# Kernel tuning notes

Measured on AMD Instinct MI355X. Metric: run time of the kernel, lower is better.

The kernel has to match this reference:

```python
import jax, jax.numpy as jnp
import numpy as np

EPS_ROT = 1e-6
EPS_FRAME = 1e-8


def make_rotX(angs):
    # angs: [..., 2] (cos-like, sin-like); returns [..., 4, 4]
    n = jnp.sqrt(jnp.sum(angs * angs, axis=-1)) + EPS_ROT
    c = angs[..., 0] / n
    s = angs[..., 1] / n
    z = jnp.zeros_like(c)
    o = jnp.ones_like(c)
    rows = jnp.stack([o, z, z, z,
                      z, c, -s, z,
                      z, s, c, z,
                      z, z, z, o], axis=-1)
    return rows.reshape(c.shape + (4, 4))


def make_rotZ(angs):
    n = jnp.sqrt(jnp.sum(angs * angs, axis=-1)) + EPS_ROT
    c = angs[..., 0] / n
    s = angs[..., 1] / n
    z = jnp.zeros_like(c)
    o = jnp.ones_like(c)
    rows = jnp.stack([c, -s, z, z,
                      s, c, z, z,
                      z, z, o, z,
                      z, z, z, o], axis=-1)
    return rows.reshape(c.shape + (4, 4))


def make_rot_axis(angs, u):
    # Rodrigues rotation about unit axis u, as homogeneous 4x4
    n = jnp.sqrt(jnp.sum(angs * angs, axis=-1)) + EPS_ROT
    ct = angs[..., 0] / n
    st = angs[..., 1] / n
    u0, u1, u2 = u[..., 0], u[..., 1], u[..., 2]
    omc = 1.0 - ct
    z = jnp.zeros_like(ct)
    o = jnp.ones_like(ct)
    rows = jnp.stack([
        ct + u0 * u0 * omc, u0 * u1 * omc - u2 * st, u0 * u2 * omc + u1 * st, z,
        u0 * u1 * omc + u2 * st, ct + u1 * u1 * omc, u1 * u2 * omc - u0 * st, z,
        u0 * u2 * omc - u1 * st, u1 * u2 * omc + u0 * st, ct + u2 * u2 * omc, z,
        z, z, z, o], axis=-1)
    return rows.reshape(ct.shape + (4, 4))


def rigid_from_3_points(N, Ca, C):
    # Gram-Schmidt backbone frame (ideal geometry branch)
    v1 = C - Ca
    v2 = N - Ca
    e1 = v1 / (jnp.linalg.norm(v1, axis=-1, keepdims=True) + EPS_FRAME)
    u2 = v2 - e1 * jnp.sum(e1 * v2, axis=-1, keepdims=True)
    e2 = u2 / (jnp.linalg.norm(u2, axis=-1, keepdims=True) + EPS_FRAME)
    e3 = jnp.cross(e1, e2)
    R = jnp.stack([e1, e2, e3], axis=-1)  # columns -> [B,L,3,3]
    return R, Ca


def _compute(seq, xyz, alphas, base_indices, RTs_in_base_frame, xyzs_in_base_frame):
    B, L = xyz.shape[:2]
    Rs, Ts = rigid_from_3_points(xyz[..., 0, :], xyz[..., 1, :], xyz[..., 2, :])
    top = jnp.concatenate([Rs, Ts[..., None]], axis=-1)  # [B,L,3,4]
    bot = jnp.broadcast_to(jnp.array([0.0, 0.0, 0.0, 1.0], dtype=xyz.dtype), (B, L, 1, 4))
    RTF0 = jnp.concatenate([top, bot], axis=-2)  # [B,L,4,4]

    RT_base = RTs_in_base_frame[seq]  # [B,L,7,4,4]

    RTF1 = RTF0 @ RT_base[:, :, 0] @ make_rotX(alphas[:, :, 0, :])
    RTF2 = RTF0 @ RT_base[:, :, 1] @ make_rotX(alphas[:, :, 1, :])
    RTF3 = RTF0 @ RT_base[:, :, 2] @ make_rotX(alphas[:, :, 2, :])

    basexyzs = xyzs_in_base_frame[seq]  # [B,L,36,4]
    NCr = 0.5 * (basexyzs[:, :, 2, :3] + basexyzs[:, :, 0, :3])
    CAr = basexyzs[:, :, 1, :3]
    CBr = basexyzs[:, :, 4, :3]
    ax1 = jnp.cross(CBr - CAr, NCr - CAr)
    ax1 = ax1 / (jnp.linalg.norm(ax1, axis=-1, keepdims=True) + 1e-8)
    NCp = basexyzs[:, :, 2, :3] - basexyzs[:, :, 0, :3]
    NCpp = NCp - jnp.sum(NCp * NCr, axis=-1, keepdims=True) / jnp.sum(NCr * NCr, axis=-1, keepdims=True) * NCr
    ax2 = jnp.cross(CBr - CAr, NCpp)
    ax2 = ax2 / (jnp.linalg.norm(ax2, axis=-1, keepdims=True) + 1e-8)

    CBrot1 = make_rot_axis(alphas[:, :, 7, :], ax1)
    CBrot2 = make_rot_axis(alphas[:, :, 8, :], ax2)
    RTF8 = RTF0 @ CBrot1 @ CBrot2

    RTF4 = RTF8 @ RT_base[:, :, 3] @ make_rotX(alphas[:, :, 3, :]) @ make_rotZ(alphas[:, :, 9, :])
    RTF5 = RTF4 @ RT_base[:, :, 4] @ make_rotX(alphas[:, :, 4, :])
    RTF6 = RTF5 @ RT_base[:, :, 5] @ make_rotX(alphas[:, :, 5, :])
    RTF7 = RTF6 @ RT_base[:, :, 6] @ make_rotX(alphas[:, :, 6, :])

    RTframes = jnp.stack([RTF0, RTF1, RTF2, RTF3, RTF4, RTF5, RTF6, RTF7, RTF8], axis=2)  # [B,L,9,4,4]

    idx = base_indices[seq]  # [B,L,36], values in [0,9)
    frames = jnp.take_along_axis(RTframes, idx[..., None, None], axis=2)  # [B,L,36,4,4]
    xyzs = jnp.einsum('blaij,blaj->blai', frames, basexyzs)
    return RTframes, xyzs[..., :3]


def setup_inputs() -> dict:
    key = jax.random.key(0)
    ks = jax.random.split(key, 6)
    B, L, NAA, NATOMS = 4, 8192, 80, 36
    seq = jax.random.randint(ks[0], (B, L), 0, NAA)
    xyz = jax.random.normal(ks[1], (B, L, 3, 3), jnp.float32)
    alphas = jax.random.normal(ks[2], (B, L, 10, 2), jnp.float32)
    base_indices = jax.random.randint(ks[3], (NAA, NATOMS), 0, 9)
    xibf = jax.random.normal(ks[4], (NAA, NATOMS, 4), jnp.float32)
    xibf = xibf.at[..., 3].set(1.0)  # homogeneous coords
    RTs = jax.random.normal(ks[5], (NAA, 7, 4, 4), jnp.float32)
    return {"seq": seq, "xyz": xyz, "alphas": alphas, "base_indices": base_indices,
            "RTs_in_base_frame": RTs, "xyzs_in_base_frame": xibf}


def reference(seq, xyz, alphas, base_indices, RTs_in_base_frame, xyzs_in_base_frame):
    return _compute(seq, xyz, alphas, base_indices, RTs_in_base_frame, xyzs_in_base_frame)
```

## Files before the change

### kernel.cpp

```cpp
#include <hip/hip_runtime.h>

#define EPS_ROT   1e-6f
#define EPS_FRAME 1e-8f

#define RPB 64
#define FRS 20
#define RSS (9*FRS)
#define PSTR 36


__device__ __forceinline__ void angNorm(float x, float y, float& c, float& s) {
    float n = sqrtf(x*x + y*y) + EPS_ROT;
    c = x / n; s = y / n;
}

__device__ __forceinline__ void loadMat4(const float* __restrict__ p, float B[4][4]) {
    const float4* q = reinterpret_cast<const float4*>(p);
#pragma unroll
    for (int i = 0; i < 4; ++i) {
        float4 r = q[i];
        B[i][0] = r.x; B[i][1] = r.y; B[i][2] = r.z; B[i][3] = r.w;
    }
}

__device__ __forceinline__ void storeMatLDS(float* dst, const float M[4][4]) {
#pragma unroll
    for (int i = 0; i < 4; ++i)
        *reinterpret_cast<float4*>(dst + i*4) = make_float4(M[i][0], M[i][1], M[i][2], M[i][3]);
}

__device__ __forceinline__ void affineMul(const float a[3][4], const float B[4][4], float C[4][4]) {
#pragma unroll
    for (int i = 0; i < 3; ++i)
#pragma unroll
        for (int j = 0; j < 4; ++j)
            C[i][j] = a[i][0]*B[0][j] + a[i][1]*B[1][j] + a[i][2]*B[2][j] + a[i][3]*B[3][j];
#pragma unroll
    for (int j = 0; j < 4; ++j) C[3][j] = B[3][j];
}

__device__ __forceinline__ void mat4Mul(const float A[4][4], const float B[4][4], float C[4][4]) {
#pragma unroll
    for (int i = 0; i < 4; ++i)
#pragma unroll
        for (int j = 0; j < 4; ++j)
            C[i][j] = A[i][0]*B[0][j] + A[i][1]*B[1][j] + A[i][2]*B[2][j] + A[i][3]*B[3][j];
}

__device__ __forceinline__ void postRotX(float M[4][4], float c, float s) {
#pragma unroll
    for (int i = 0; i < 4; ++i) {
        float m1 = M[i][1], m2 = M[i][2];
        M[i][1] = c*m1 + s*m2;
        M[i][2] = c*m2 - s*m1;
    }
}

__device__ __forceinline__ void rotAxis3(float G[3][3], float c, float s,
                                         float u0, float u1, float u2) {
    float omc = 1.0f - c;
    G[0][0] = c + u0*u0*omc;    G[0][1] = u0*u1*omc - u2*s; G[0][2] = u0*u2*omc + u1*s;
    G[1][0] = u0*u1*omc + u2*s; G[1][1] = c + u1*u1*omc;    G[1][2] = u1*u2*omc - u0*s;
    G[2][0] = u0*u2*omc - u1*s; G[2][1] = u1*u2*omc + u0*s; G[2][2] = c + u2*u2*omc;
}

__device__ __forceinline__ void mat3Mul(const float A[3][3], const float B[3][3], float C[3][3]) {
#pragma unroll
    for (int i = 0; i < 3; ++i)
#pragma unroll
        for (int j = 0; j < 3; ++j)
            C[i][j] = A[i][0]*B[0][j] + A[i][1]*B[1][j] + A[i][2]*B[2][j];
}

__device__ __forceinline__ void computeF0(const float* __restrict__ xyz, int t, float f0[3][4]) {
    const float* p = xyz + (size_t)t * 9;
    float N0=p[0], N1=p[1], N2=p[2];
    float A0=p[3], A1=p[4], A2=p[5];
    float C0=p[6], C1=p[7], C2=p[8];

    float v10=C0-A0, v11=C1-A1, v12=C2-A2;
    float v20=N0-A0, v21=N1-A1, v22=N2-A2;
    float n1 = sqrtf(v10*v10 + v11*v11 + v12*v12) + EPS_FRAME;
    float e10=v10/n1, e11=v11/n1, e12=v12/n1;
    float d  = e10*v20 + e11*v21 + e12*v22;
    float u20=v20-e10*d, u21=v21-e11*d, u22=v22-e12*d;
    float n2 = sqrtf(u20*u20 + u21*u21 + u22*u22) + EPS_FRAME;
    float e20=u20/n2, e21=u21/n2, e22=u22/n2;
    float e30=e11*e22 - e12*e21;
    float e31=e12*e20 - e10*e22;
    float e32=e10*e21 - e11*e20;

    f0[0][0]=e10; f0[0][1]=e20; f0[0][2]=e30; f0[0][3]=A0;
    f0[1][0]=e11; f0[1][1]=e21; f0[1][2]=e31; f0[1][3]=A1;
    f0[2][0]=e12; f0[2][1]=e22; f0[2][2]=e32; f0[2][3]=A2;
}


__global__ __launch_bounds__(256) void fused_kernel(
    const int*   __restrict__ seq,
    const float* __restrict__ xyz,
    const float* __restrict__ alphas,
    const int*   __restrict__ bidx,
    const float* __restrict__ RTs,
    const float* __restrict__ xibf,
    float*       __restrict__ out_fr,
    float*       __restrict__ out_xyz,
    int BL)
{
    __shared__ float lds_fr[RPB * RSS];
    __shared__ float lds_P[RPB * PSTR];
    __shared__ int   lds_seq[RPB];

    const int tid = threadIdx.x;
    const int wv  = tid >> 6;
    const int r   = tid & 63;
    const int base = blockIdx.x * RPB;
    const int t   = base + r;
    const bool valid = (t < BL);

    int s = 0;
    if (valid) s = seq[t];
    const float* rb = RTs + (size_t)s * 112;
    const float* al = alphas + (size_t)t * 20;
    float* fl = lds_fr + r * RSS;

    float f8[3][4];
    float P6[4][4], P7[4][4];

    if (valid) {
        if (wv == 0) {
            lds_seq[r] = s;
            float f0[3][4]; computeF0(xyz, t, f0);
            float F0[4][4] = { {f0[0][0],f0[0][1],f0[0][2],f0[0][3]},
                               {f0[1][0],f0[1][1],f0[1][2],f0[1][3]},
                               {f0[2][0],f0[2][1],f0[2][2],f0[2][3]},
                               {0.f,0.f,0.f,1.f} };
            storeMatLDS(fl + 0*FRS, F0);

            float2 a0 = *reinterpret_cast<const float2*>(al + 0);
            float c0, s0; angNorm(a0.x, a0.y, c0, s0);
            float B[4][4]; loadMat4(rb + 0, B);
            float F[4][4]; affineMul(f0, B, F); postRotX(F, c0, s0);
            storeMatLDS(fl + 1*FRS, F);
        } else if (wv == 1) {
            float f0[3][4]; computeF0(xyz, t, f0);
            float2 a1 = *reinterpret_cast<const float2*>(al + 2);
            float2 a2 = *reinterpret_cast<const float2*>(al + 4);
            float c, sn;
            float B[4][4], F[4][4];
            angNorm(a1.x, a1.y, c, sn);
            loadMat4(rb + 16, B); affineMul(f0, B, F); postRotX(F, c, sn);
            storeMatLDS(fl + 2*FRS, F);
            angNorm(a2.x, a2.y, c, sn);
            loadMat4(rb + 32, B); affineMul(f0, B, F); postRotX(F, c, sn);
            storeMatLDS(fl + 3*FRS, F);
        } else if (wv == 2) {
            float f0[3][4]; computeF0(xyz, t, f0);
            const float* bxp = xibf + (size_t)s * 144;
            float4 b0 = reinterpret_cast<const float4*>(bxp)[0];
            float4 b1 = reinterpret_cast<const float4*>(bxp)[1];
            float4 b2 = reinterpret_cast<const float4*>(bxp)[2];
            float4 b4 = reinterpret_cast<const float4*>(bxp)[4];

            float NCr0 = 0.5f*(b2.x + b0.x), NCr1 = 0.5f*(b2.y + b0.y), NCr2 = 0.5f*(b2.z + b0.z);
            float ba0 = b4.x - b1.x, ba1 = b4.y - b1.y, ba2 = b4.z - b1.z;
            float w0 = NCr0 - b1.x, w1 = NCr1 - b1.y, w2 = NCr2 - b1.z;
            float x10 = ba1*w2 - ba2*w1, x11 = ba2*w0 - ba0*w2, x12 = ba0*w1 - ba1*w0;
            float xn1 = sqrtf(x10*x10 + x11*x11 + x12*x12) + 1e-8f;
            x10 /= xn1; x11 /= xn1; x12 /= xn1;
            float NCp0 = b2.x - b0.x, NCp1 = b2.y - b0.y, NCp2 = b2.z - b0.z;
            float dp = NCp0*NCr0 + NCp1*NCr1 + NCp2*NCr2;
            float dr = NCr0*NCr0 + NCr1*NCr1 + NCr2*NCr2;
            float sf = dp / dr;
            float q0 = NCp0 - sf*NCr0, q1 = NCp1 - sf*NCr1, q2 = NCp2 - sf*NCr2;
            float x20 = ba1*q2 - ba2*q1, x21 = ba2*q0 - ba0*q2, x22 = ba0*q1 - ba1*q0;
            float xn2 = sqrtf(x20*x20 + x21*x21 + x22*x22) + 1e-8f;
            x20 /= xn2; x21 /= xn2; x22 /= xn2;

            float2 a7 = *reinterpret_cast<const float2*>(al + 14);
            float2 a8 = *reinterpret_cast<const float2*>(al + 16);
            float c7, s7, c8, s8;
            angNorm(a7.x, a7.y, c7, s7);
            angNorm(a8.x, a8.y, c8, s8);
            float G1[3][3], G2[3][3], G12[3][3], R8[3][3];
            rotAxis3(G1, c7, s7, x10, x11, x12);
            rotAxis3(G2, c8, s8, x20, x21, x22);
            mat3Mul(G1, G2, G12);
            float R0[3][3] = { {f0[0][0],f0[0][1],f0[0][2]},
                               {f0[1][0],f0[1][1],f0[1][2]},
                               {f0[2][0],f0[2][1],f0[2][2]} };
            mat3Mul(R0, G12, R8);
#pragma unroll
            for (int i = 0; i < 3; ++i) {
                f8[i][0] = R8[i][0]; f8[i][1] = R8[i][1]; f8[i][2] = R8[i][2];
                f8[i][3] = f0[i][3];
            }
            float F8[4][4] = { {f8[0][0],f8[0][1],f8[0][2],f8[0][3]},
                               {f8[1][0],f8[1][1],f8[1][2],f8[1][3]},
                               {f8[2][0],f8[2][1],f8[2][2],f8[2][3]},
                               {0.f,0.f,0.f,1.f} };
            storeMatLDS(fl + 8*FRS, F8);
        } else {
            float2 a3 = *reinterpret_cast<const float2*>(al + 6);
            float2 a4 = *reinterpret_cast<const float2*>(al + 8);
            float2 a5 = *reinterpret_cast<const float2*>(al + 10);
            float2 a6 = *reinterpret_cast<const float2*>(al + 12);
            float2 a9 = *reinterpret_cast<const float2*>(al + 18);
            float c3,s3, c4,s4, c5,s5, c6,s6, c9,s9;
            angNorm(a3.x, a3.y, c3, s3);
            angNorm(a4.x, a4.y, c4, s4);
            angNorm(a5.x, a5.y, c5, s5);
            angNorm(a6.x, a6.y, c6, s6);
            angNorm(a9.x, a9.y, c9, s9);

            float M00 = c9,     M01 = -s9;
            float M10 = c3*s9,  M11 = c3*c9,  M12 = -s3;
            float M20 = s3*s9,  M21 = s3*c9,  M22 = c3;

            float B[4][4]; loadMat4(rb + 48, B);
            float P4[4][4];
#pragma unroll
            for (int i = 0; i < 4; ++i) {
                P4[i][0] = B[i][0]*M00 + B[i][1]*M10 + B[i][2]*M20;
                P4[i][1] = B[i][0]*M01 + B[i][1]*M11 + B[i][2]*M21;
                P4[i][2] =               B[i][1]*M12 + B[i][2]*M22;
                P4[i][3] = B[i][3];
            }
            float P5[4][4];
            loadMat4(rb + 64, B); mat4Mul(P4, B, P5); postRotX(P5, c4, s4);
            loadMat4(rb + 80, B); mat4Mul(P5, B, P6); postRotX(P6, c5, s5);
            loadMat4(rb + 96, B); mat4Mul(P6, B, P7); postRotX(P7, c6, s6);

            float* pl = lds_P + r * PSTR;
            storeMatLDS(pl,      P4);
            storeMatLDS(pl + 16, P5);
        }
    }
    __syncthreads();

    if (valid) {
        if (wv == 2) {
            const float* pl = lds_P + r * PSTR;
            float P[4][4], F[4][4];
            loadMat4(pl, P);
            affineMul(f8, P, F); storeMatLDS(fl + 4*FRS, F);
            loadMat4(pl + 16, P);
            affineMul(f8, P, F); storeMatLDS(fl + 5*FRS, F);
        } else if (wv == 3) {
            float f8b[3][4];
            const float* q = fl + 8*FRS;
#pragma unroll
            for (int i = 0; i < 3; ++i) {
                float4 v = *reinterpret_cast<const float4*>(q + i*4);
                f8b[i][0] = v.x; f8b[i][1] = v.y; f8b[i][2] = v.z; f8b[i][3] = v.w;
            }
            float F[4][4];
            affineMul(f8b, P6, F); storeMatLDS(fl + 6*FRS, F);
            affineMul(f8b, P7, F); storeMatLDS(fl + 7*FRS, F);
        }
    }
    __syncthreads();

    for (int c = tid; c < RPB*36; c += 256) {
        int res = c / 36;
        int q = c - res*36;
        int tt = base + res;
        if (tt < BL) {
            float4 v = *reinterpret_cast<const float4*>(
                lds_fr + res*RSS + (q >> 2)*FRS + (q & 3)*4);
            *reinterpret_cast<float4*>(out_fr + (size_t)tt*144 + q*4) = v;
        }
    }

    for (int c = tid; c < RPB*36; c += 256) {
        int res = c / 36;
        int a = c - res*36;
        int tt = base + res;
        if (tt < BL) {
            int ss = lds_seq[res];
            int idx = bidx[ss*36 + a];
            const float* fp = lds_fr + res*RSS + idx*FRS;
            float4 r0 = *reinterpret_cast<const float4*>(fp);
            float4 r1 = *reinterpret_cast<const float4*>(fp + 4);
            float4 r2 = *reinterpret_cast<const float4*>(fp + 8);
            float4 v  = *reinterpret_cast<const float4*>(xibf + ((size_t)ss*36 + a)*4);
            size_t o = (size_t)tt*108 + (size_t)a*3;
            out_xyz[o+0] = r0.x*v.x + r0.y*v.y + r0.z*v.z + r0.w*v.w;
            out_xyz[o+1] = r1.x*v.x + r1.y*v.y + r1.z*v.z + r1.w*v.w;
            out_xyz[o+2] = r2.x*v.x + r2.y*v.y + r2.z*v.z + r2.w*v.w;
        }
    }
}


extern "C" void kernel_launch(void* const* d_in, const int* in_sizes, int n_in,
                              void* d_out, int out_size, void* d_ws, size_t ws_size,
                              hipStream_t stream) {
    const int*   seq    = (const int*)  d_in[0];
    const float* xyz    = (const float*)d_in[1];
    const float* alphas = (const float*)d_in[2];
    const int*   bidx   = (const int*)  d_in[3];
    const float* RTs    = (const float*)d_in[4];
    const float* xibf   = (const float*)d_in[5];
    float*       out    = (float*)d_out;

    int BL = in_sizes[0];
    float* out_xyz = out + (size_t)BL * 144;

    int blocks = (BL + RPB - 1) / RPB;
    fused_kernel<<<blocks, 256, 0, stream>>>(seq, xyz, alphas, bidx, RTs, xibf,
                                             out, out_xyz, BL);
}
```

Before: 16.54 us.

## Coalesce xyz output stores, shrink LDS frame stride, use rsqrt normalization

Rewrites the atom-coordinate write loop so each thread produces one output float, giving contiguous coalesced stores instead of three strided scalar writes per thread. It also stores both output arrays with nontemporal stores and shrinks the per-frame LDS stride from 20 to 18 floats, which forces float2 LDS accesses. The P4/P5 staging buffer is dropped so wave 3 computes all four composed frames itself, and launch bounds request 3 blocks per CU. Normalizations switch from sqrt-plus-epsilon divides to a clamped rsqrt, which changes the epsilon semantics slightly and may cause small numerical differences.

```diff
diff --git a/kernel.cpp b/kernel.cpp
--- a/kernel.cpp
+++ b/kernel.cpp
@@ -1,32 +1,44 @@
 #include <hip/hip_runtime.h>
 
-#define EPS_ROT   1e-6f
-#define EPS_FRAME 1e-8f
-
 #define RPB 64
-#define FRS 20
+#define FRS 18
 #define RSS (9*FRS)
-#define PSTR 36
-
+
+typedef float __attribute__((ext_vector_type(4))) fvec4;
+
+
+__device__ __forceinline__ float rsqz(float d) { return rsqrtf(fmaxf(d, 1e-24f)); }
 
 __device__ __forceinline__ void angNorm(float x, float y, float& c, float& s) {
-    float n = sqrtf(x*x + y*y) + EPS_ROT;
-    c = x / n; s = y / n;
+    float inv = rsqz(x*x + y*y);
+    c = x * inv; s = y * inv;
 }
 
 __device__ __forceinline__ void loadMat4(const float* __restrict__ p, float B[4][4]) {
-    const float4* q = reinterpret_cast<const float4*>(p);
+    const float4* q4 = reinterpret_cast<const float4*>(p);
 #pragma unroll
     for (int i = 0; i < 4; ++i) {
-        float4 r = q[i];
-        B[i][0] = r.x; B[i][1] = r.y; B[i][2] = r.z; B[i][3] = r.w;
-    }
+        float4 r = q4[i];
+        B[i][0]=r.x; B[i][1]=r.y; B[i][2]=r.z; B[i][3]=r.w;
+    }
+}
+
+__device__ __forceinline__ void storeRowLDS(float* dst, float a, float b, float c, float d) {
+    *reinterpret_cast<float2*>(dst)     = make_float2(a, b);
+    *reinterpret_cast<float2*>(dst + 2) = make_float2(c, d);
 }
 
 __device__ __forceinline__ void storeMatLDS(float* dst, const float M[4][4]) {
 #pragma unroll
     for (int i = 0; i < 4; ++i)
-        *reinterpret_cast<float4*>(dst + i*4) = make_float4(M[i][0], M[i][1], M[i][2], M[i][3]);
+        storeRowLDS(dst + i*4, M[i][0], M[i][1], M[i][2], M[i][3]);
+}
+
+__device__ __forceinline__ void storeAffineLDS(float* dst, const float f[3][4]) {
+#pragma unroll
+    for (int i = 0; i < 3; ++i)
+        storeRowLDS(dst + i*4, f[i][0], f[i][1], f[i][2], f[i][3]);
+    storeRowLDS(dst + 12, 0.f, 0.f, 0.f, 1.f);
 }
 
 __device__ __forceinline__ void affineMul(const float a[3][4], const float B[4][4], float C[4][4]) {
@@ -80,12 +92,12 @@
 
     float v10=C0-A0, v11=C1-A1, v12=C2-A2;
     float v20=N0-A0, v21=N1-A1, v22=N2-A2;
-    float n1 = sqrtf(v10*v10 + v11*v11 + v12*v12) + EPS_FRAME;
-    float e10=v10/n1, e11=v11/n1, e12=v12/n1;
+    float i1 = rsqz(v10*v10 + v11*v11 + v12*v12);
+    float e10=v10*i1, e11=v11*i1, e12=v12*i1;
     float d  = e10*v20 + e11*v21 + e12*v22;
     float u20=v20-e10*d, u21=v21-e11*d, u22=v22-e12*d;
-    float n2 = sqrtf(u20*u20 + u21*u21 + u22*u22) + EPS_FRAME;
-    float e20=u20/n2, e21=u21/n2, e22=u22/n2;
+    float i2 = rsqz(u20*u20 + u21*u21 + u22*u22);
+    float e20=u20*i2, e21=u21*i2, e22=u22*i2;
     float e30=e11*e22 - e12*e21;
     float e31=e12*e20 - e10*e22;
     float e32=e10*e21 - e11*e20;
@@ -96,7 +108,7 @@
 }
 
 
-__global__ __launch_bounds__(256) void fused_kernel(
+__global__ __launch_bounds__(256, 3) void fused_kernel(
     const int*   __restrict__ seq,
     const float* __restrict__ xyz,
     const float* __restrict__ alphas,
@@ -108,14 +120,13 @@
     int BL)
 {
     __shared__ float lds_fr[RPB * RSS];
-    __shared__ float lds_P[RPB * PSTR];
     __shared__ int   lds_seq[RPB];
 
-    const int tid = threadIdx.x;
-    const int wv  = tid >> 6;
-    const int r   = tid & 63;
+    const int tid  = threadIdx.x;
+    const int wv   = tid >> 6;
+    const int r    = tid & 63;
     const int base = blockIdx.x * RPB;
-    const int t   = base + r;
+    const int t    = base + r;
     const bool valid = (t < BL);
 
     int s = 0;
@@ -124,23 +135,19 @@
     const float* al = alphas + (size_t)t * 20;
     float* fl = lds_fr + r * RSS;
 
-    float f8[3][4];
-    float P6[4][4], P7[4][4];
+    float P4[4][4], P5[4][4], P6[4][4], P7[4][4];
 
     if (valid) {
         if (wv == 0) {
             lds_seq[r] = s;
             float f0[3][4]; computeF0(xyz, t, f0);
-            float F0[4][4] = { {f0[0][0],f0[0][1],f0[0][2],f0[0][3]},
-                               {f0[1][0],f0[1][1],f0[1][2],f0[1][3]},
-                               {f0[2][0],f0[2][1],f0[2][2],f0[2][3]},
-                               {0.f,0.f,0.f,1.f} };
-            storeMatLDS(fl + 0*FRS, F0);
+            storeAffineLDS(fl, f0);
 
             float2 a0 = *reinterpret_cast<const float2*>(al + 0);
             float c0, s0; angNorm(a0.x, a0.y, c0, s0);
-            float B[4][4]; loadMat4(rb + 0, B);
-            float F[4][4]; affineMul(f0, B, F); postRotX(F, c0, s0);
+            float B[4][4], F[4][4];
+            loadMat4(rb + 0, B);
+            affineMul(f0, B, F); postRotX(F, c0, s0);
             storeMatLDS(fl + 1*FRS, F);
         } else if (wv == 1) {
             float f0[3][4]; computeF0(xyz, t, f0);
@@ -166,16 +173,16 @@
             float ba0 = b4.x - b1.x, ba1 = b4.y - b1.y, ba2 = b4.z - b1.z;
             float w0 = NCr0 - b1.x, w1 = NCr1 - b1.y, w2 = NCr2 - b1.z;
             float x10 = ba1*w2 - ba2*w1, x11 = ba2*w0 - ba0*w2, x12 = ba0*w1 - ba1*w0;
-            float xn1 = sqrtf(x10*x10 + x11*x11 + x12*x12) + 1e-8f;
-            x10 /= xn1; x11 /= xn1; x12 /= xn1;
+            float in1 = rsqz(x10*x10 + x11*x11 + x12*x12);
+            x10 *= in1; x11 *= in1; x12 *= in1;
             float NCp0 = b2.x - b0.x, NCp1 = b2.y - b0.y, NCp2 = b2.z - b0.z;
             float dp = NCp0*NCr0 + NCp1*NCr1 + NCp2*NCr2;
             float dr = NCr0*NCr0 + NCr1*NCr1 + NCr2*NCr2;
             float sf = dp / dr;
             float q0 = NCp0 - sf*NCr0, q1 = NCp1 - sf*NCr1, q2 = NCp2 - sf*NCr2;
             float x20 = ba1*q2 - ba2*q1, x21 = ba2*q0 - ba0*q2, x22 = ba0*q1 - ba1*q0;
-            float xn2 = sqrtf(x20*x20 + x21*x21 + x22*x22) + 1e-8f;
-            x20 /= xn2; x21 /= xn2; x22 /= xn2;
+            float in2 = rsqz(x20*x20 + x21*x21 + x22*x22);
+            x20 *= in2; x21 *= in2; x22 *= in2;
 
             float2 a7 = *reinterpret_cast<const float2*>(al + 14);
             float2 a8 = *reinterpret_cast<const float2*>(al + 16);
@@ -190,16 +197,13 @@
                                {f0[1][0],f0[1][1],f0[1][2]},
                                {f0[2][0],f0[2][1],f0[2][2]} };
             mat3Mul(R0, G12, R8);
+            float f8[3][4];
 #pragma unroll
             for (int i = 0; i < 3; ++i) {
                 f8[i][0] = R8[i][0]; f8[i][1] = R8[i][1]; f8[i][2] = R8[i][2];
                 f8[i][3] = f0[i][3];
             }
-            float F8[4][4] = { {f8[0][0],f8[0][1],f8[0][2],f8[0][3]},
-                               {f8[1][0],f8[1][1],f8[1][2],f8[1][3]},
-                               {f8[2][0],f8[2][1],f8[2][2],f8[2][3]},
-                               {0.f,0.f,0.f,1.f} };
-            storeMatLDS(fl + 8*FRS, F8);
+            storeAffineLDS(fl + 8*FRS, f8);
         } else {
             float2 a3 = *reinterpret_cast<const float2*>(al + 6);
             float2 a4 = *reinterpret_cast<const float2*>(al + 8);
@@ -213,12 +217,12 @@
             angNorm(a6.x, a6.y, c6, s6);
             angNorm(a9.x, a9.y, c9, s9);
 
-            float M00 = c9,     M01 = -s9;
-            float M10 = c3*s9,  M11 = c3*c9,  M12 = -s3;
-            float M20 = s3*s9,  M21 = s3*c9,  M22 = c3;
-
-            float B[4][4]; loadMat4(rb + 48, B);
-            float P4[4][4];
+            float M00 = c9,    M01 = -s9;
+            float M10 = c3*s9, M11 = c3*c9, M12 = -s3;
+            float M20 = s3*s9, M21 = s3*c9, M22 = c3;
+
+            float B[4][4];
+            loadMat4(rb + 48, B);
 #pragma unroll
             for (int i = 0; i < 4; ++i) {
                 P4[i][0] = B[i][0]*M00 + B[i][1]*M10 + B[i][2]*M20;
@@ -226,68 +230,63 @@
                 P4[i][2] =               B[i][1]*M12 + B[i][2]*M22;
                 P4[i][3] = B[i][3];
             }
-            float P5[4][4];
             loadMat4(rb + 64, B); mat4Mul(P4, B, P5); postRotX(P5, c4, s4);
             loadMat4(rb + 80, B); mat4Mul(P5, B, P6); postRotX(P6, c5, s5);
             loadMat4(rb + 96, B); mat4Mul(P6, B, P7); postRotX(P7, c6, s6);
-
-            float* pl = lds_P + r * PSTR;
-            storeMatLDS(pl,      P4);
-            storeMatLDS(pl + 16, P5);
         }
     }
     __syncthreads();
 
-    if (valid) {
-        if (wv == 2) {
-            const float* pl = lds_P + r * PSTR;
-            float P[4][4], F[4][4];
-            loadMat4(pl, P);
-            affineMul(f8, P, F); storeMatLDS(fl + 4*FRS, F);
-            loadMat4(pl + 16, P);
-            affineMul(f8, P, F); storeMatLDS(fl + 5*FRS, F);
-        } else if (wv == 3) {
-            float f8b[3][4];
-            const float* q = fl + 8*FRS;
-#pragma unroll
-            for (int i = 0; i < 3; ++i) {
-                float4 v = *reinterpret_cast<const float4*>(q + i*4);
-                f8b[i][0] = v.x; f8b[i][1] = v.y; f8b[i][2] = v.z; f8b[i][3] = v.w;
-            }
-            float F[4][4];
-            affineMul(f8b, P6, F); storeMatLDS(fl + 6*FRS, F);
-            affineMul(f8b, P7, F); storeMatLDS(fl + 7*FRS, F);
+    if (valid && wv == 3) {
+        float f8b[3][4];
+        const float* qp = fl + 8*FRS;
+#pragma unroll
+        for (int i = 0; i < 3; ++i) {
+            float2 u = *reinterpret_cast<const float2*>(qp + i*4);
+            float2 w = *reinterpret_cast<const float2*>(qp + i*4 + 2);
+            f8b[i][0]=u.x; f8b[i][1]=u.y; f8b[i][2]=w.x; f8b[i][3]=w.y;
         }
+        float F[4][4];
+        affineMul(f8b, P4, F); storeMatLDS(fl + 4*FRS, F);
+        affineMul(f8b, P5, F); storeMatLDS(fl + 5*FRS, F);
+        affineMul(f8b, P6, F); storeMatLDS(fl + 6*FRS, F);
+        affineMul(f8b, P7, F); storeMatLDS(fl + 7*FRS, F);
     }
     __syncthreads();
 
-    for (int c = tid; c < RPB*36; c += 256) {
+#pragma unroll
+    for (int k = 0; k < 9; ++k) {
+        int c = tid + k*256;
         int res = c / 36;
         int q = c - res*36;
         int tt = base + res;
         if (tt < BL) {
-            float4 v = *reinterpret_cast<const float4*>(
-                lds_fr + res*RSS + (q >> 2)*FRS + (q & 3)*4);
-            *reinterpret_cast<float4*>(out_fr + (size_t)tt*144 + q*4) = v;
+            const float* p = lds_fr + res*RSS + (q >> 2)*FRS + (q & 3)*4;
+            float2 u = *reinterpret_cast<const float2*>(p);
+            float2 w = *reinterpret_cast<const float2*>(p + 2);
+            fvec4 v4 = { u.x, u.y, w.x, w.y };
+            __builtin_nontemporal_store(v4,
+                reinterpret_cast<fvec4*>(out_fr) + (size_t)tt*36 + q);
         }
     }
 
-    for (int c = tid; c < RPB*36; c += 256) {
-        int res = c / 36;
-        int a = c - res*36;
+#pragma unroll
+    for (int k = 0; k < 27; ++k) {
+        int c = tid + k*256;
+        int res = c / 108;
+        int rem = c - res*108;
+        int a   = rem / 3;
+        int row = rem - a*3;
         int tt = base + res;
         if (tt < BL) {
-            int ss = lds_seq[res];
+            int ss  = lds_seq[res];
             int idx = bidx[ss*36 + a];
-            const float* fp = lds_fr + res*RSS + idx*FRS;
-            float4 r0 = *reinterpret_cast<const float4*>(fp);
-            float4 r1 = *reinterpret_cast<const float4*>(fp + 4);
-            float4 r2 = *reinterpret_cast<const float4*>(fp + 8);
-            float4 v  = *reinterpret_cast<const float4*>(xibf + ((size_t)ss*36 + a)*4);
-            size_t o = (size_t)tt*108 + (size_t)a*3;
-            out_xyz[o+0] = r0.x*v.x + r0.y*v.y + r0.z*v.z + r0.w*v.w;
-            out_xyz[o+1] = r1.x*v.x + r1.y*v.y + r1.z*v.z + r1.w*v.w;
-            out_xyz[o+2] = r2.x*v.x + r2.y*v.y + r2.z*v.z + r2.w*v.w;
+            const float* fp = lds_fr + res*RSS + idx*FRS + row*4;
+            float2 u = *reinterpret_cast<const float2*>(fp);
+            float2 w = *reinterpret_cast<const float2*>(fp + 2);
+            float4 v = *reinterpret_cast<const float4*>(xibf + ((size_t)ss*36 + a)*4);
+            float val = u.x*v.x + u.y*v.y + w.x*v.z + w.y*v.w;
+            __builtin_nontemporal_store(val, out_xyz + (size_t)base*108 + c);
         }
     }
 }
```

Result: slower. 18.17 us (+9.8%).
